# Kernel optimization log

Hardware: AMD Instinct MI355X
Metric: run time of the kernel (lower is better)

Reference implementation:

```python
import jax, jax.numpy as jnp
import numpy as np

T, H, E, K = 4096, 1024, 8, 2
DFF = 4 * H


def setup_inputs() -> dict:
    key = jax.random.key(0)
    ks = jax.random.split(key, 5)
    scale_in = 1.0 / np.sqrt(H)
    scale_ff = 1.0 / np.sqrt(DFF)
    return {
        "x": jax.random.normal(ks[0], (T, H), dtype=jnp.float32),
        "gate_w": jax.random.normal(ks[1], (H, E), dtype=jnp.float32) * scale_in,
        "gate_b": jnp.zeros((E,), dtype=jnp.float32),
        "w1": jax.random.normal(ks[2], (E, H, DFF), dtype=jnp.float32) * scale_in,
        "b1": jnp.zeros((E, DFF), dtype=jnp.float32),
        "w2": jax.random.normal(ks[3], (E, DFF, H), dtype=jnp.float32) * scale_ff,
        "b2": jnp.zeros((E, H), dtype=jnp.float32),
    }


def _aux_loss(probs, indices):
    # importance loss: torch.var uses unbiased (ddof=1)
    importance = probs.sum(0)                                  # [E]
    importance_loss = jnp.var(importance, ddof=1) / (E ** 2)
    # mask[t,e] = True if expert e is among token t's top-k
    mask = jax.nn.one_hot(indices, E, dtype=probs.dtype).sum(1)  # [T,E] in {0,1}
    routing_probs = probs * mask
    expert_usage = mask.mean(0)                                # [E]
    routing_weights = routing_probs.mean(0)                    # [E]
    load_balance_loss = E * (expert_usage * routing_weights).sum()
    return importance_loss + load_balance_loss


def reference(x, gate_w, gate_b, w1, b1, w2, b2):
    # gate + routing
    logits = x @ gate_w + gate_b                               # [T,E]
    probs = jax.nn.softmax(logits, axis=-1)
    weights, indices = jax.lax.top_k(probs, K)                 # [T,K], [T,K]
    aux_loss = _aux_loss(probs, indices)

    # expert MLPs + combine. Reference computes each expert densely over all
    # tokens and masks by routing weight (E is small & fixed); this matches the
    # gather/compute/scatter math exactly: out[t] = sum_k weights[t,k] * MLP_{e(t,k)}(x[t]).
    out = jnp.zeros((T, H), dtype=x.dtype)
    for e in range(E):
        gate_e = (weights * (indices == e)).sum(-1)            # [T]
        h = jax.nn.relu(x @ w1[e] + b1[e])                     # [T,4H]
        y = h @ w2[e] + b2[e]                                  # [T,H]
        out = out + gate_e[:, None] * y
    return out, aux_loss
```

## Files before the change

kernel.cpp:

```cpp
#include <hip/hip_runtime.h>
#include <stdint.h>

#define T_TOK 4096
#define H_DIM 1024
#define E_EXP 8
#define DFF_D 4096
#define HROWS 10240
#define NT 40
#define G1_ITEMS 640
#define TR2_ITEMS 2048
#define GATE_BLKS 512
#define TR1_ITEMS 2048

typedef __attribute__((ext_vector_type(4))) float f32x4;
typedef __attribute__((ext_vector_type(8))) __bf16 bf16x8;

static __device__ __forceinline__ unsigned short f2bf(float f) {
  union { float f; unsigned u; } v; v.f = f;
  unsigned r = v.u + 0x7FFFu + ((v.u >> 16) & 1u);
  return (unsigned short)(r >> 16);
}
static __device__ __forceinline__ float bf2f(unsigned short u) {
  union { unsigned u; float f; } v; v.u = ((unsigned)u) << 16; return v.f;
}
static __device__ __forceinline__ void load_lds16(const void* g, void* l) {
  __builtin_amdgcn_global_load_lds(
      (const __attribute__((address_space(1))) unsigned int*)g,
      (__attribute__((address_space(3))) unsigned int*)l, 16, 0, 0);
}

#define MEMF() asm volatile("" ::: "memory")
#define BAR()  { MEMF(); __builtin_amdgcn_s_barrier(); MEMF(); }
#define VM4()  asm volatile("s_waitcnt vmcnt(4)" ::: "memory")
#define VM2()  asm volatile("s_waitcnt vmcnt(2)" ::: "memory")
#define VM0()  asm volatile("s_waitcnt vmcnt(0)" ::: "memory")
#define SP1()  __builtin_amdgcn_s_setprio(1)
#define SP0()  __builtin_amdgcn_s_setprio(0)

static __device__ __forceinline__ void tr_tile_to_tiled(
    unsigned short* __restrict__ tile16,
    const float* __restrict__ src, int src_ld,
    int r0, int c0,
    unsigned short* __restrict__ tile_out,
    int tid) {
  const int w = tid >> 6, lane = tid & 63;
#pragma unroll
  for (int i = 0; i < 8; ++i) {
    const int row = w * 8 + i;
    float4 v = *(const float4*)&src[(size_t)(r0 + row) * src_ld + c0 + 4 * lane];
    ushort4 o;
    o.x = f2bf(v.x); o.y = f2bf(v.y); o.z = f2bf(v.z); o.w = f2bf(v.w);
    *(ushort4*)&tile16[row * 260 + 4 * lane] = o;
  }
  __syncthreads();
  const int r0t = ((tid >> 7) << 4) + ((tid >> 2) & 15);
  const int kbt = (((tid >> 6) & 1) << 5) + (((tid & 3) << 3) ^ (((tid >> 5) & 1) << 4));
#pragma unroll
  for (int half = 0; half < 2; ++half)
#pragma unroll
    for (int j = 0; j < 2; ++j) {
      const int c = half * 128 + 64 * j + r0t;
      unsigned ow[4];
#pragma unroll
      for (int p = 0; p < 4; ++p)
        ow[p] = (unsigned)tile16[(kbt + 2 * p) * 260 + c]
              | ((unsigned)tile16[(kbt + 2 * p + 1) * 260 + c] << 16);
      *(uint4*)((char*)tile_out + half * 16384 + j * 8192 + tid * 16) = *(uint4*)ow;
    }
}

__global__ __launch_bounds__(512) void gate_tr1_kernel(
    const float* __restrict__ x, const float* __restrict__ gw,
    const float* __restrict__ gb,
    int* __restrict__ counts,
    int* __restrict__ entry_token, float* __restrict__ entry_gate,
    int* __restrict__ ids, int* __restrict__ slots,
    float* __restrict__ partials,
    unsigned short* __restrict__ xb,
    const float* __restrict__ w1, unsigned short* __restrict__ w1t) {
  extern __shared__ char smem[];
  const int tid = threadIdx.x;
  const int blk = blockIdx.x;

  if (blk >= GATE_BLKS) {
    const int j = blk - GATE_BLKS;
    const int e2 = j >> 8;
    const int jj = j & 255;
    const int nt = jj >> 4, kt = jj & 15;
    tr_tile_to_tiled((unsigned short*)smem,
                     w1 + (size_t)e2 * H_DIM * DFF_D, DFF_D,
                     kt * 64, nt * 256,
                     w1t + ((size_t)((e2 * 16 + nt) * 16 + kt)) * 16384,
                     tid);
    return;
  }

  float (*probs_lds)[8] = (float(*)[8])smem;
  int   (*topi_lds)[2]  = (int(*)[2])(smem + 256);
  const int lane = tid & 63, tl = tid >> 6;
  const int token = blk * 8 + tl;
  float a[8];
#pragma unroll
  for (int e = 0; e < 8; ++e) a[e] = 0.f;
#pragma unroll
  for (int i = 0; i < 4; ++i) {
    const int k4 = i * 256 + lane * 4;
    float4 xv4 = *(const float4*)&x[(size_t)token * H_DIM + k4];
    ushort4 xo;
    xo.x = f2bf(xv4.x); xo.y = f2bf(xv4.y); xo.z = f2bf(xv4.z); xo.w = f2bf(xv4.w);
    *(ushort4*)&xb[(size_t)token * H_DIM + k4] = xo;
#pragma unroll
    for (int j = 0; j < 4; ++j) {
      const float xv = ((const float*)&xv4)[j];
      const float4* g = (const float4*)&gw[(size_t)(k4 + j) * 8];
      float4 g0 = g[0], g1 = g[1];
      a[0] += xv * g0.x; a[1] += xv * g0.y; a[2] += xv * g0.z; a[3] += xv * g0.w;
      a[4] += xv * g1.x; a[5] += xv * g1.y; a[6] += xv * g1.z; a[7] += xv * g1.w;
    }
  }
  for (int m = 32; m >= 1; m >>= 1) {
#pragma unroll
    for (int e = 0; e < 8; ++e) a[e] += __shfl_xor(a[e], m);
  }
  if (lane == 0) {
    float lg[8], p[8];
    float mx = -1e30f;
#pragma unroll
    for (int e = 0; e < 8; ++e) { lg[e] = a[e] + gb[e]; mx = lg[e] > mx ? lg[e] : mx; }
    float s = 0.f;
#pragma unroll
    for (int e = 0; e < 8; ++e) { p[e] = expf(lg[e] - mx); s += p[e]; }
    float inv = 1.f / s;
#pragma unroll
    for (int e = 0; e < 8; ++e) p[e] *= inv;
    int i0 = 0;
#pragma unroll
    for (int e = 1; e < 8; ++e) if (p[e] > p[i0]) i0 = e;
    int i1 = (i0 == 0) ? 1 : 0;
#pragma unroll
    for (int e = 0; e < 8; ++e) if (e != i0 && p[e] > p[i1]) i1 = e;
#pragma unroll
    for (int e = 0; e < 8; ++e) probs_lds[tl][e] = p[e];
    topi_lds[tl][0] = i0; topi_lds[tl][1] = i1;
    int s0 = atomicAdd(&counts[i0], 1);
    entry_token[i0 * T_TOK + s0] = token;
    entry_gate[i0 * T_TOK + s0] = p[i0];
    ids[token * 2] = i0; slots[token * 2] = s0;
    int s1 = atomicAdd(&counts[i1], 1);
    entry_token[i1 * T_TOK + s1] = token;
    entry_gate[i1 * T_TOK + s1] = p[i1];
    ids[token * 2 + 1] = i1; slots[token * 2 + 1] = s1;
  }
  __syncthreads();
  if (tid < 24) {
    int e = tid & 7, which = tid >> 3;
    float s = 0.f;
#pragma unroll
    for (int tt = 0; tt < 8; ++tt) {
      float pv = probs_lds[tt][e];
      bool m = (topi_lds[tt][0] == e) || (topi_lds[tt][1] == e);
      if (which == 0) s += pv;
      else if (which == 1) s += m ? 1.f : 0.f;
      else s += m ? pv : 0.f;
    }
    partials[blk * 24 + tid] = s;
  }
}

__global__ void meta_kernel(const int* __restrict__ counts, const float* __restrict__ partials,
                            int* __restrict__ hoff, int* __restrict__ tmap,
                            float* __restrict__ out_aux) {
  __shared__ float red[24][33];
  const int tid = threadIdx.x;
  if (tid == 0) {
    int o = 0, nt = 0;
    for (int e = 0; e < E_EXP; ++e) {
      hoff[e] = o;
      int rtc = (counts[e] + 255) >> 8;
      o += rtc << 8;
      for (int rt = 0; rt < rtc; ++rt) tmap[nt++] = (e << 16) | rt;
    }
    hoff[E_EXP] = o;
    for (; nt < NT; ++nt) tmap[nt] = -1;
  }
  const int c = tid & 31, g = tid >> 5;
  if (c < 24) {
    float s = 0.f;
    for (int j = 0; j < 16; ++j) s += partials[(size_t)(g + j * 32) * 24 + c];
    red[c][g] = s;
  }
  __syncthreads();
  if (tid < 24) {
    float t2 = 0.f;
#pragma unroll
    for (int g2 = 0; g2 < 32; ++g2) t2 += red[tid][g2];
    red[tid][32] = t2;
  }
  __syncthreads();
  if (tid == 0) {
    float mean = 0.f;
    for (int e = 0; e < 8; ++e) mean += red[e][32];
    mean *= 0.125f;
    float var = 0.f;
    for (int e = 0; e < 8; ++e) { float d = red[e][32] - mean; var += d * d; }
    var *= (1.f / 7.f);
    float il = var * (1.f / 64.f);
    float lb = 0.f;
    for (int e = 0; e < 8; ++e)
      lb += (red[8 + e][32] / (float)T_TOK) * (red[16 + e][32] / (float)T_TOK);
    lb *= 8.f;
    out_aux[0] = il + lb;
  }
}

#define STG_A0(m_) { char* lb_ = sA + ((m_)&1)*32768 + wv*1024; \
  load_lds16(pa0s0 + (size_t)(m_)*128, lb_); load_lds16(pa0s1 + (size_t)(m_)*128, lb_ + 8192); }
#define STG_A1(m_) { char* lb_ = sA + ((m_)&1)*32768 + 16384 + wv*1024; \
  load_lds16(pa1s0 + (size_t)(m_)*128, lb_); load_lds16(pa1s1 + (size_t)(m_)*128, lb_ + 8192); }
#define STG_B0(m_) { char* lb_ = sB + ((m_)&1)*32768 + wv*1024; \
  load_lds16(pb0s0 + (size_t)(m_)*32768, lb_); load_lds16(pb0s1 + (size_t)(m_)*32768, lb_ + 8192); }
#define STG_B1(m_) { char* lb_ = sB + ((m_)&1)*32768 + 16384 + wv*1024; \
  load_lds16(pb1s0 + (size_t)(m_)*32768, lb_); load_lds16(pb1s1 + (size_t)(m_)*32768, lb_ + 8192); }

#define LDA8(DST, AD) \
  _Pragma("unroll") for (int mi = 0; mi < 4; ++mi) \
  _Pragma("unroll") for (int kk = 0; kk < 2; ++kk) \
    DST[mi][kk] = *(const bf16x8*)((AD) + (amfrag + mi) * 2048 + kk * 1024 + lane_off);
#define LDB4(DST, BD) \
  _Pragma("unroll") for (int ni = 0; ni < 2; ++ni) \
  _Pragma("unroll") for (int kk = 0; kk < 2; ++kk) \
    DST[ni][kk] = *(const bf16x8*)((BD) + (bnfrag + ni) * 2048 + kk * 1024 + lane_off);
#define MF16(ACC, AF, BF) \
  _Pragma("unroll") for (int mi = 0; mi < 4; ++mi) \
  _Pragma("unroll") for (int ni = 0; ni < 2; ++ni) \
  _Pragma("unroll") for (int kk = 0; kk < 2; ++kk) \
    ACC[mi][ni] = __builtin_amdgcn_mfma_f32_16x16x32_bf16(AF[mi][kk], BF[ni][kk], ACC[mi][ni], 0, 0, 0);

#define ACC_INIT() \
  f32x4 q00[4][2], q01[4][2], q10[4][2], q11[4][2]; \
  _Pragma("unroll") for (int mi = 0; mi < 4; ++mi) \
  _Pragma("unroll") for (int ni = 0; ni < 2; ++ni) { \
    q00[mi][ni] = (f32x4){0.f,0.f,0.f,0.f}; q01[mi][ni] = (f32x4){0.f,0.f,0.f,0.f}; \
    q10[mi][ni] = (f32x4){0.f,0.f,0.f,0.f}; q11[mi][ni] = (f32x4){0.f,0.f,0.f,0.f}; }

#define PROLOGUE() \
  STG_A0(0); STG_B0(0); STG_B1(0); STG_A1(0); \
  VM0(); \
  BAR();

#define KLOOP_DEEP(KT) \
  for (int k = 0; k < (KT); ++k) { \
    const char* Ab = sA + (k & 1) * 32768; \
    const char* Bb = sB + (k & 1) * 32768; \
    bf16x8 alo[4][2], ahi[4][2], blo[2][2], bhi[2][2]; \
    LDA8(alo, Ab); LDB4(blo, Bb); \
    if (k + 1 < (KT)) STG_A0(k + 1); \
    BAR(); \
    SP1(); MF16(q00, alo, blo); SP0(); \
    if (k + 1 < (KT)) { VM4(); } else { VM2(); } \
    BAR(); \
    LDB4(bhi, Bb + 16384); \
    if (k + 1 < (KT)) STG_B0(k + 1); \
    BAR(); \
    SP1(); MF16(q01, alo, bhi); SP0(); \
    if (k + 1 < (KT)) { VM4(); } else { VM0(); } \
    BAR(); \
    LDA8(ahi, Ab + 16384); \
    if (k + 1 < (KT)) STG_B1(k + 1); \
    BAR(); \
    SP1(); MF16(q10, ahi, blo); SP0(); \
    BAR(); \
    if (k + 1 < (KT)) STG_A1(k + 1); \
    BAR(); \
    SP1(); MF16(q11, ahi, bhi); SP0(); \
    VM4(); \
    BAR(); \
  }

__global__ __launch_bounds__(512, 2) void gemm1_kernel(
    const unsigned short* __restrict__ xb,
    const unsigned short* __restrict__ w1t,
    const float* __restrict__ b1,
    const int* __restrict__ counts, const int* __restrict__ hoff,
    const int* __restrict__ tmap, const int* __restrict__ entry_token,
    unsigned short* __restrict__ h,
    const float* __restrict__ w2,
    unsigned short* __restrict__ w2t)
{
  extern __shared__ char smem[];
  char* sA = smem;
  char* sB = smem + 65536;
  const int tid = threadIdx.x;
  const int item = blockIdx.x;

  if (item >= G1_ITEMS) {
    const int j = item - G1_ITEMS;
    const int e2 = j >> 8;
    const int jj = j & 255;
    const int nt = jj >> 6, kt = jj & 63;
    tr_tile_to_tiled((unsigned short*)smem,
                     w2 + (size_t)e2 * DFF_D * H_DIM, H_DIM,
                     kt * 64, nt * 256,
                     w2t + ((size_t)((e2 * 4 + nt) * 64 + kt)) * 16384,
                     tid);
    return;
  }

  int* tok = (int*)(smem + 131072);
  int lin = item;
  lin = (lin & 7) * (G1_ITEMS / 8) + (lin >> 3);
  const int ti = lin % NT, ct = lin / NT;
  const int mEnc = tmap[ti];
  if (mEnc < 0) return;
  const int e = mEnc >> 16, rt = mEnc & 0xffff;
  const int cnt = counts[e];
  const int lane = tid & 63, wv = tid >> 6;
  if (tid < 256) {
    int s = rt * 256 + tid;
    if (s >= cnt) s = cnt - 1;
    tok[tid] = entry_token[e * T_TOK + s];
  }
  __syncthreads();
  const int r0 = ((tid >> 7) << 4) + ((tid >> 2) & 15);
  const int kb = (((tid >> 6) & 1) << 5) + (((tid & 3) << 3) ^ (((tid >> 5) & 1) << 4));
  const char* xbb = (const char*)xb;
  const char* pa0s0 = xbb + (size_t)tok[r0]       * 2048 + kb * 2;
  const char* pa0s1 = xbb + (size_t)tok[64 + r0]  * 2048 + kb * 2;
  const char* pa1s0 = xbb + (size_t)tok[128 + r0] * 2048 + kb * 2;
  const char* pa1s1 = xbb + (size_t)tok[192 + r0] * 2048 + kb * 2;
  const char* w1e = (const char*)w1t + ((size_t)(e * 16 + ct) * 16) * 32768;
  const char* pb0s0 = w1e + tid * 16;
  const char* pb0s1 = w1e + 8192 + tid * 16;
  const char* pb1s0 = w1e + 16384 + tid * 16;
  const char* pb1s1 = w1e + 24576 + tid * 16;
  const int amfrag = (wv >> 2) * 4;
  const int bnfrag = (wv & 3) * 2;
  const int mb0 = (wv >> 2) * 64, nb0 = (wv & 3) * 32;
  const int lane_off = (lane & 15) * 64 + ((((lane >> 4) << 3) ^ (((lane >> 3) & 1) << 4)) << 1);
  ACC_INIT()
  PROLOGUE()
  KLOOP_DEEP(16)
  const int rb = hoff[e] + rt * 256;
  const float* b1e = b1 + (size_t)e * DFF_D;
#define EPI1(ACC, A_, B_) \
  _Pragma("unroll") for (int mi = 0; mi < 4; ++mi) \
  _Pragma("unroll") for (int ni = 0; ni < 2; ++ni) { \
    const int n = ct * 256 + (B_) * 128 + nb0 + ni * 16 + (lane & 15); \
    const float bias = b1e[n]; \
    _Pragma("unroll") for (int q = 0; q < 4; ++q) { \
      const int m = (A_) * 128 + mb0 + mi * 16 + (lane >> 4) * 4 + q; \
      float v = ACC[mi][ni][q] + bias; v = v > 0.f ? v : 0.f; \
      h[(size_t)(rb + m) * DFF_D + n] = f2bf(v); \
    } }
  EPI1(q00, 0, 0) EPI1(q01, 0, 1) EPI1(q10, 1, 0) EPI1(q11, 1, 1)
#undef EPI1
}

__global__ __launch_bounds__(512, 2) void gemm2_kernel(
    const unsigned short* __restrict__ h,
    const unsigned short* __restrict__ w2t,
    const float* __restrict__ b2,
    const int* __restrict__ hoff, const int* __restrict__ tmap,
    const float* __restrict__ entry_gate,
    unsigned short* __restrict__ yp)
{
  extern __shared__ char smem[];
  char* sA = smem;
  char* sB = smem + 65536;
  int lin = (blockIdx.z * NT + blockIdx.y) * 4 + blockIdx.x;
  lin = (lin & 7) * (3 * NT * 4 / 8) + (lin >> 3);
  const int ct = lin & 3;
  const int g = lin >> 2;
  const int ti = g % NT, part = g / NT;
  const int mEnc = tmap[ti];
  if (mEnc < 0) return;
  const int e = mEnc >> 16, rt = mEnc & 0xffff;
  int S, KT;
  if (part == 0)      { S = 0;  KT = 22; }
  else if (part == 1) { S = 22; KT = 21; }
  else                { S = 43; KT = 21; }
  const int tid = threadIdx.x, lane = tid & 63, wv = tid >> 6;
  const int rb = hoff[e] + rt * 256;
  const int r0 = ((tid >> 7) << 4) + ((tid >> 2) & 15);
  const int kb = (((tid >> 6) & 1) << 5) + (((tid & 3) << 3) ^ (((tid >> 5) & 1) << 4));
  const char* hb = (const char*)h + (size_t)S * 128;
  const char* pa0s0 = hb + (size_t)(rb + r0)       * 8192 + kb * 2;
  const char* pa0s1 = hb + (size_t)(rb + 64 + r0)  * 8192 + kb * 2;
  const char* pa1s0 = hb + (size_t)(rb + 128 + r0) * 8192 + kb * 2;
  const char* pa1s1 = hb + (size_t)(rb + 192 + r0) * 8192 + kb * 2;
  const char* w2e = (const char*)w2t + ((size_t)((e * 4 + ct) * 64 + S)) * 32768;
  const char* pb0s0 = w2e + tid * 16;
  const char* pb0s1 = w2e + 8192 + tid * 16;
  const char* pb1s0 = w2e + 16384 + tid * 16;
  const char* pb1s1 = w2e + 24576 + tid * 16;
  const int amfrag = (wv >> 2) * 4;
  const int bnfrag = (wv & 3) * 2;
  const int mb0 = (wv >> 2) * 64, nb0 = (wv & 3) * 32;
  const int lane_off = (lane & 15) * 64 + ((((lane >> 4) << 3) ^ (((lane >> 3) & 1) << 4)) << 1);
  ACC_INIT()
  PROLOGUE()
  KLOOP_DEEP(KT)
  unsigned short* yout = yp + (size_t)part * HROWS * H_DIM;
  const float* b2e = b2 + (size_t)e * H_DIM;
  const float* ge = entry_gate + (size_t)e * T_TOK + rt * 256;
#define EPI2(ACC, A_, B_) \
  _Pragma("unroll") for (int mi = 0; mi < 4; ++mi) \
  _Pragma("unroll") for (int ni = 0; ni < 2; ++ni) { \
    const int n = ct * 256 + (B_) * 128 + nb0 + ni * 16 + (lane & 15); \
    const float bias = (part == 0) ? b2e[n] : 0.f; \
    _Pragma("unroll") for (int q = 0; q < 4; ++q) { \
      const int m = (A_) * 128 + mb0 + mi * 16 + (lane >> 4) * 4 + q; \
      const float gate = ge[m];   \
      float v = (ACC[mi][ni][q] + bias) * gate; \
      yout[(size_t)(rb + m) * H_DIM + n] = f2bf(v); \
    } }
  EPI2(q00, 0, 0) EPI2(q01, 0, 1) EPI2(q10, 1, 0) EPI2(q11, 1, 1)
#undef EPI2
}

__global__ void combine_kernel(const unsigned short* __restrict__ yp,
                               const int* __restrict__ ids, const int* __restrict__ slots,
                               const int* __restrict__ hoff, float* __restrict__ out) {
  const int t = blockIdx.x, tid = threadIdx.x;
  const int r0 = hoff[ids[t * 2]] + slots[t * 2];
  const int r1 = hoff[ids[t * 2 + 1]] + slots[t * 2 + 1];
  const int c = tid * 4;
  float4 o = {0.f, 0.f, 0.f, 0.f};
#pragma unroll
  for (int p = 0; p < 3; ++p) {
    const unsigned short* pl = yp + (size_t)p * HROWS * H_DIM;
    ushort4 a = *(const ushort4*)&pl[(size_t)r0 * H_DIM + c];
    ushort4 b = *(const ushort4*)&pl[(size_t)r1 * H_DIM + c];
    o.x += bf2f(a.x) + bf2f(b.x);
    o.y += bf2f(a.y) + bf2f(b.y);
    o.z += bf2f(a.z) + bf2f(b.z);
    o.w += bf2f(a.w) + bf2f(b.w);
  }
  *(float4*)&out[(size_t)t * H_DIM + c] = o;
}

__global__ void ws_fail_kernel(float* out) {
  if (threadIdx.x == 0 && blockIdx.x == 0) out[0] = -12345.0f;
}

#define XB_OFF    ((size_t)0)
#define W1T_OFF   ((size_t)8388608)
#define YP_OFF    ((size_t)0)
#define W2T_OFF   ((size_t)75497472)
#define H_OFF     ((size_t)142606336)
#define TMAP_OFF  ((size_t)226492416)
#define ET_OFF    ((size_t)226492672)
#define EG_OFF    ((size_t)226623744)
#define IDS_OFF   ((size_t)226754816)
#define SLOT_OFF  ((size_t)226787584)
#define CNT_OFF   ((size_t)226820352)
#define HOFF_OFF  ((size_t)226820416)
#define PART_OFF  ((size_t)226820480)
#define WS_NEED   ((size_t)226918784)

extern "C" void kernel_launch(void* const* d_in, const int* in_sizes, int n_in,
                              void* d_out, int out_size, void* d_ws, size_t ws_size,
                              hipStream_t stream) {
  const float* x  = (const float*)d_in[0];
  const float* gw = (const float*)d_in[1];
  const float* gb = (const float*)d_in[2];
  const float* w1 = (const float*)d_in[3];
  const float* b1 = (const float*)d_in[4];
  const float* w2 = (const float*)d_in[5];
  const float* b2 = (const float*)d_in[6];
  float* out = (float*)d_out;
  char* ws = (char*)d_ws;

  if (ws_size < WS_NEED) {
    ws_fail_kernel<<<1, 64, 0, stream>>>(out);
    return;
  }

  unsigned short* xb  = (unsigned short*)(ws + XB_OFF);
  unsigned short* w1t = (unsigned short*)(ws + W1T_OFF);
  unsigned short* yp  = (unsigned short*)(ws + YP_OFF);
  unsigned short* w2t = (unsigned short*)(ws + W2T_OFF);
  unsigned short* h   = (unsigned short*)(ws + H_OFF);
  int*   tmap  = (int*)(ws + TMAP_OFF);
  int*   etok  = (int*)(ws + ET_OFF);
  float* egate = (float*)(ws + EG_OFF);
  int*   ids   = (int*)(ws + IDS_OFF);
  int*   slots = (int*)(ws + SLOT_OFF);
  int*   counts= (int*)(ws + CNT_OFF);
  int*   hoff  = (int*)(ws + HOFF_OFF);
  float* parts = (float*)(ws + PART_OFF);

  hipMemsetAsync(counts, 0, 32, stream);

  gate_tr1_kernel<<<GATE_BLKS + TR1_ITEMS, 512, 33280, stream>>>(
      x, gw, gb, counts, etok, egate, ids, slots, parts, xb, w1, w1t);
  meta_kernel<<<1, 1024, 0, stream>>>(counts, parts, hoff, tmap, out + (size_t)T_TOK * H_DIM);
  gemm1_kernel<<<G1_ITEMS + TR2_ITEMS, 512, 132096, stream>>>(
      xb, w1t, b1, counts, hoff, tmap, etok, h, w2, w2t);
  gemm2_kernel<<<dim3(4, NT, 3), 512, 131072, stream>>>(h, w2t, b2, hoff, tmap, egate, yp);
  combine_kernel<<<4096, 256, 0, stream>>>(yp, ids, slots, hoff, out);
}
```

Measured before the change: 356.6 us.

## Replace global atomic expert routing with per-block counts and prefix-scan slot assignment

The gate kernel no longer uses global atomicAdd on per-expert counters. Each block now records its local per-expert counts and the intra-block position of each token, and the single-block meta kernel runs a prefix scan over block counts to compute deterministic slots and scatter the entry lists. The fused gate+w1-transpose launch is split into two separate launches, and the counts memset is dropped. This removes atomic contention and makes the routing order deterministic, at the cost of an extra launch and more serial work in the one-block meta kernel.

```diff
diff --git a/kernel.cpp b/kernel.cpp
--- a/kernel.cpp
+++ b/kernel.cpp
@@ -9,7 +9,6 @@
 #define NT 40
 #define G1_ITEMS 640
 #define TR2_ITEMS 2048
-#define GATE_BLKS 512
 #define TR1_ITEMS 2048
 
 typedef __attribute__((ext_vector_type(4))) float f32x4;
@@ -19,6 +18,9 @@
   union { float f; unsigned u; } v; v.f = f;
   unsigned r = v.u + 0x7FFFu + ((v.u >> 16) & 1u);
   return (unsigned short)(r >> 16);
+}
+static __device__ __forceinline__ unsigned pack2bf(float a, float b) {
+  return (unsigned)f2bf(a) | ((unsigned)f2bf(b) << 16);
 }
 static __device__ __forceinline__ float bf2f(unsigned short u) {
   union { unsigned u; float f; } v; v.u = ((unsigned)u) << 16; return v.f;
@@ -69,34 +71,33 @@
     }
 }
 
-__global__ __launch_bounds__(512) void gate_tr1_kernel(
+__global__ __launch_bounds__(512) void tr1_kernel(const float* __restrict__ w1,
+                                                  unsigned short* __restrict__ w1t) {
+  extern __shared__ char smem[];
+  const int j = blockIdx.x;
+  const int e2 = j >> 8;
+  const int jj = j & 255;
+  const int nt = jj >> 4, kt = jj & 15;
+  tr_tile_to_tiled((unsigned short*)smem,
+                   w1 + (size_t)e2 * H_DIM * DFF_D, DFF_D,
+                   kt * 64, nt * 256,
+                   w1t + ((size_t)((e2 * 16 + nt) * 16 + kt)) * 16384,
+                   threadIdx.x);
+}
+
+__global__ __launch_bounds__(512) void gate_kernel(
     const float* __restrict__ x, const float* __restrict__ gw,
     const float* __restrict__ gb,
-    int* __restrict__ counts,
-    int* __restrict__ entry_token, float* __restrict__ entry_gate,
-    int* __restrict__ ids, int* __restrict__ slots,
+    int* __restrict__ ids, int* __restrict__ locs, float* __restrict__ tokg,
+    int* __restrict__ bcnt,
     float* __restrict__ partials,
-    unsigned short* __restrict__ xb,
-    const float* __restrict__ w1, unsigned short* __restrict__ w1t) {
-  extern __shared__ char smem[];
+    unsigned short* __restrict__ xb) {
+  __shared__ float probs_lds[8][8];
+  __shared__ int   topi_lds[8][2];
+  __shared__ int   locs_lds[16];
+  __shared__ int   cnt_lds[8];
   const int tid = threadIdx.x;
   const int blk = blockIdx.x;
-
-  if (blk >= GATE_BLKS) {
-    const int j = blk - GATE_BLKS;
-    const int e2 = j >> 8;
-    const int jj = j & 255;
-    const int nt = jj >> 4, kt = jj & 15;
-    tr_tile_to_tiled((unsigned short*)smem,
-                     w1 + (size_t)e2 * H_DIM * DFF_D, DFF_D,
-                     kt * 64, nt * 256,
-                     w1t + ((size_t)((e2 * 16 + nt) * 16 + kt)) * 16384,
-                     tid);
-    return;
-  }
-
-  float (*probs_lds)[8] = (float(*)[8])smem;
-  int   (*topi_lds)[2]  = (int(*)[2])(smem + 256);
   const int lane = tid & 63, tl = tid >> 6;
   const int token = blk * 8 + tl;
   float a[8];
@@ -142,16 +143,29 @@
 #pragma unroll
     for (int e = 0; e < 8; ++e) probs_lds[tl][e] = p[e];
     topi_lds[tl][0] = i0; topi_lds[tl][1] = i1;
-    int s0 = atomicAdd(&counts[i0], 1);
-    entry_token[i0 * T_TOK + s0] = token;
-    entry_gate[i0 * T_TOK + s0] = p[i0];
-    ids[token * 2] = i0; slots[token * 2] = s0;
-    int s1 = atomicAdd(&counts[i1], 1);
-    entry_token[i1 * T_TOK + s1] = token;
-    entry_gate[i1 * T_TOK + s1] = p[i1];
-    ids[token * 2 + 1] = i1; slots[token * 2 + 1] = s1;
-  }
-  __syncthreads();
+  }
+  __syncthreads();
+  if (tid == 0) {
+    int run[8];
+#pragma unroll
+    for (int e = 0; e < 8; ++e) run[e] = 0;
+    for (int q = 0; q < 16; ++q) {
+      const int e = topi_lds[q >> 1][q & 1];
+      locs_lds[q] = run[e]++;
+    }
+#pragma unroll
+    for (int e = 0; e < 8; ++e) cnt_lds[e] = run[e];
+  }
+  __syncthreads();
+  if (tid < 16) {
+    const int tt = tid >> 1, c = tid & 1;
+    const int t2 = blk * 8 + tt;
+    const int e = topi_lds[tt][c];
+    ids[t2 * 2 + c]  = e;
+    locs[t2 * 2 + c] = locs_lds[tid];
+    tokg[t2 * 2 + c] = probs_lds[tt][e];
+  }
+  if (tid >= 16 && tid < 24) bcnt[blk * 8 + (tid - 16)] = cnt_lds[tid - 16];
   if (tid < 24) {
     int e = tid & 7, which = tid >> 3;
     float s = 0.f;
@@ -167,21 +181,62 @@
   }
 }
 
-__global__ void meta_kernel(const int* __restrict__ counts, const float* __restrict__ partials,
-                            int* __restrict__ hoff, int* __restrict__ tmap,
-                            float* __restrict__ out_aux) {
+__global__ __launch_bounds__(1024) void meta_kernel(
+    const int* __restrict__ bcnt, const int* __restrict__ ids,
+    const int* __restrict__ locs, const float* __restrict__ tokg,
+    const float* __restrict__ partials,
+    int* __restrict__ counts, int* __restrict__ hoff, int* __restrict__ tmap,
+    int* __restrict__ entry_token, float* __restrict__ entry_gate,
+    int* __restrict__ slots, float* __restrict__ out_aux) {
+  __shared__ int sc[8][513];
   __shared__ float red[24][33];
   const int tid = threadIdx.x;
+#pragma unroll
+  for (int j = 0; j < 4; ++j) {
+    const int idx = tid + j * 1024;
+    const int e = idx >> 9, b = idx & 511;
+    sc[e][b] = bcnt[b * 8 + e];
+  }
+  __syncthreads();
+  for (int off = 1; off < 512; off <<= 1) {
+    int v[4];
+#pragma unroll
+    for (int j = 0; j < 4; ++j) {
+      const int idx = tid + j * 1024;
+      const int e = idx >> 9, b = idx & 511;
+      v[j] = sc[e][b] + (b >= off ? sc[e][b - off] : 0);
+    }
+    __syncthreads();
+#pragma unroll
+    for (int j = 0; j < 4; ++j) {
+      const int idx = tid + j * 1024;
+      sc[idx >> 9][idx & 511] = v[j];
+    }
+    __syncthreads();
+  }
   if (tid == 0) {
     int o = 0, nt = 0;
     for (int e = 0; e < E_EXP; ++e) {
+      const int ce = sc[e][511];
+      counts[e] = ce;
       hoff[e] = o;
-      int rtc = (counts[e] + 255) >> 8;
+      int rtc = (ce + 255) >> 8;
       o += rtc << 8;
       for (int rt = 0; rt < rtc; ++rt) tmap[nt++] = (e << 16) | rt;
     }
     hoff[E_EXP] = o;
     for (; nt < NT; ++nt) tmap[nt] = -1;
+  }
+  __syncthreads();
+#pragma unroll
+  for (int j = 0; j < 8; ++j) {
+    const int idx = tid + j * 1024;
+    const int t = idx >> 1, c = idx & 1, b = t >> 3;
+    const int e = ids[t * 2 + c];
+    const int slot = sc[e][b] - bcnt[b * 8 + e] + locs[t * 2 + c];
+    entry_token[e * T_TOK + slot] = t;
+    entry_gate[e * T_TOK + slot] = tokg[t * 2 + c];
+    slots[t * 2 + c] = slot;
   }
   const int c = tid & 31, g = tid >> 5;
   if (c < 24) {
@@ -456,7 +511,10 @@
 #define CNT_OFF   ((size_t)226820352)
 #define HOFF_OFF  ((size_t)226820416)
 #define PART_OFF  ((size_t)226820480)
-#define WS_NEED   ((size_t)226918784)
+#define BCNT_OFF  ((size_t)226918784)
+#define LOCS_OFF  ((size_t)226935168)
+#define TOKG_OFF  ((size_t)226967936)
+#define WS_NEED   ((size_t)227000704)
 
 extern "C" void kernel_launch(void* const* d_in, const int* in_sizes, int n_in,
                               void* d_out, int out_size, void* d_ws, size_t ws_size,
@@ -489,12 +547,15 @@
   int*   counts= (int*)(ws + CNT_OFF);
   int*   hoff  = (int*)(ws + HOFF_OFF);
   float* parts = (float*)(ws + PART_OFF);
-
-  hipMemsetAsync(counts, 0, 32, stream);
-
-  gate_tr1_kernel<<<GATE_BLKS + TR1_ITEMS, 512, 33280, stream>>>(
-      x, gw, gb, counts, etok, egate, ids, slots, parts, xb, w1, w1t);
-  meta_kernel<<<1, 1024, 0, stream>>>(counts, parts, hoff, tmap, out + (size_t)T_TOK * H_DIM);
+  int*   bcnt  = (int*)(ws + BCNT_OFF);
+  int*   locs  = (int*)(ws + LOCS_OFF);
+  float* tokg  = (float*)(ws + TOKG_OFF);
+
+  gate_kernel<<<512, 512, 0, stream>>>(x, gw, gb, ids, locs, tokg, bcnt, parts, xb);
+  tr1_kernel<<<TR1_ITEMS, 512, 33280, stream>>>(w1, w1t);
+  meta_kernel<<<1, 1024, 0, stream>>>(bcnt, ids, locs, tokg, parts,
+                                      counts, hoff, tmap, etok, egate, slots,
+                                      out + (size_t)T_TOK * H_DIM);
   gemm1_kernel<<<G1_ITEMS + TR2_ITEMS, 512, 132096, stream>>>(
       xb, w1t, b1, counts, hoff, tmap, etok, h, w2, w2t);
   gemm2_kernel<<<dim3(4, NT, 3), 512, 131072, stream>>>(h, w2t, b2, hoff, tmap, egate, yp);
```

After: 294.1 us. 1.21x faster.
